# Optimization experiments

Measured on AMD Instinct MI355X. Metric: run time of the kernel, lower is better.

The kernel has to match this reference:

```python
import jax, jax.numpy as jnp
import numpy as np

B, L, D, H, I = 4, 1024, 2048, 16, 8192
DH = D // H  # 128
EPS = 1e-6


def setup_inputs() -> dict:
    key = jax.random.key(0)
    ks = jax.random.split(key, 10)
    hidden_states = jax.random.normal(ks[0], (B, L, D), dtype=jnp.float32)
    # additive causal mask [B,1,L,L]: 0 on allowed, large negative on masked
    causal = jnp.tril(jnp.ones((L, L), dtype=bool))
    attention_mask = jnp.where(causal, 0.0, -1e9).astype(jnp.float32)
    attention_mask = jnp.broadcast_to(attention_mask[None, None], (B, 1, L, L))
    # RoPE tables [B,L,DH]
    inv_freq = 1.0 / (10000.0 ** (jnp.arange(0, DH, 2, dtype=jnp.float32) / DH))
    pos = jnp.arange(L, dtype=jnp.float32)
    freqs = pos[:, None] * inv_freq[None, :]            # [L, DH/2]
    emb = jnp.concatenate([freqs, freqs], axis=-1)       # [L, DH]
    cos = jnp.broadcast_to(jnp.cos(emb)[None], (B, L, DH)).astype(jnp.float32)
    sin = jnp.broadcast_to(jnp.sin(emb)[None], (B, L, DH)).astype(jnp.float32)
    s = 0.02
    return {
        "hidden_states": hidden_states,
        "attention_mask": attention_mask,
        "cos": cos,
        "sin": sin,
        "q_w": jax.random.normal(ks[1], (D, D), jnp.float32) * s,
        "k_w": jax.random.normal(ks[2], (D, D), jnp.float32) * s,
        "v_w": jax.random.normal(ks[3], (D, D), jnp.float32) * s,
        "o_w": jax.random.normal(ks[4], (D, D), jnp.float32) * s,
        "gate_w": jax.random.normal(ks[5], (I, D), jnp.float32) * s,
        "up_w": jax.random.normal(ks[6], (I, D), jnp.float32) * s,
        "down_w": jax.random.normal(ks[7], (D, I), jnp.float32) * s,
        "ln1_w": jnp.ones((D,), jnp.float32),
        "ln2_w": jnp.ones((D,), jnp.float32),
    }


def _rms_norm(x, w):
    var = jnp.mean(jnp.square(x), axis=-1, keepdims=True)
    return x * jax.lax.rsqrt(var + EPS) * w


def _rotate_half(x):
    x1, x2 = jnp.split(x, 2, axis=-1)
    return jnp.concatenate([-x2, x1], axis=-1)


def reference(hidden_states, attention_mask, cos, sin, q_w, k_w, v_w, o_w,
              gate_w, up_w, down_w, ln1_w, ln2_w):
    residual = hidden_states
    h = _rms_norm(hidden_states, ln1_w)                       # [B,L,D]
    # QKV projections (torch Linear: x @ W^T)
    def heads(x, w):
        return (x @ w.T).reshape(B, L, H, DH).transpose(0, 2, 1, 3)  # [B,H,L,DH]
    q, k, v = heads(h, q_w), heads(h, k_w), heads(h, v_w)
    cos_b, sin_b = cos[:, None], sin[:, None]                 # [B,1,L,DH]
    q = q * cos_b + _rotate_half(q) * sin_b
    k = k * cos_b + _rotate_half(k) * sin_b
    scores = jnp.einsum('bhqd,bhkd->bhqk', q, k) / jnp.sqrt(jnp.float32(DH))
    scores = scores + attention_mask                          # [B,H,L,L]
    attn = jax.nn.softmax(scores, axis=-1)
    ctx = jnp.einsum('bhqk,bhkd->bhqd', attn, v)              # [B,H,L,DH]
    ctx = ctx.transpose(0, 2, 1, 3).reshape(B, L, D)
    attn_out = ctx @ o_w.T
    h1 = residual + attn_out
    h2 = _rms_norm(h1, ln2_w)
    mlp = (jax.nn.silu(h2 @ gate_w.T) * (h2 @ up_w.T)) @ down_w.T
    out = h1 + mlp
    return out, attn
```

## Files before the change

kernel.cpp:

```cpp
#include <hip/hip_runtime.h>


typedef __bf16 bf16;
typedef __bf16 bf16x8 __attribute__((ext_vector_type(8)));
typedef __bf16 bf16x4 __attribute__((ext_vector_type(4)));
typedef float  f32x4  __attribute__((ext_vector_type(4)));

constexpr int   kB  = 4;
constexpr int   kL  = 1024;
constexpr int   kD  = 2048;
constexpr int   kH  = 16;
constexpr int   kI  = 8192;
constexpr int   kDH = 128;
constexpr int   kQKV = 3 * kD;
constexpr float kEps = 1e-6f;
constexpr float kScoreScale = 0.08838834764831845f;

typedef __attribute__((address_space(1))) void gvoid_t;
typedef __attribute__((address_space(3))) void lvoid_t;

__device__ __forceinline__ void gload_lds16(const void* g, void* l) {
  __builtin_amdgcn_global_load_lds((gvoid_t*)g, (lvoid_t*)l, 16, 0, 0);
}

#define ASM_VMCNT(n) asm volatile("s_waitcnt vmcnt(" #n ")" ::: "memory")

__device__ __forceinline__ void bar_raw() {
  asm volatile("" ::: "memory");
  __builtin_amdgcn_s_barrier();
  asm volatile("" ::: "memory");
}

__global__ __launch_bounds__(256) void cast_f32_bf16_kernel(
    const float* __restrict__ x, bf16* __restrict__ y, long n) {
  long i = ((long)blockIdx.x * 256 + threadIdx.x) * 4;
  long stride = (long)gridDim.x * 256 * 4;
  for (; i < n; i += stride) {
    const float4 v = *reinterpret_cast<const float4*>(x + i);
    bf16x4 o;
    o[0] = (bf16)v.x; o[1] = (bf16)v.y; o[2] = (bf16)v.z; o[3] = (bf16)v.w;
    *reinterpret_cast<bf16x4*>(y + i) = o;
  }
}

__global__ __launch_bounds__(256) void rmsnorm_kernel(
    const float* __restrict__ x, const float* __restrict__ w,
    bf16* __restrict__ out) {
  const long row = blockIdx.x;
  const float* xr = x + row * (long)kD;
  bf16* orow = out + row * (long)kD;
  const int t = threadIdx.x;

  float4 v0 = *(const float4*)(xr + t * 8);
  float4 v1 = *(const float4*)(xr + t * 8 + 4);
  float ss = v0.x * v0.x + v0.y * v0.y + v0.z * v0.z + v0.w * v0.w +
             v1.x * v1.x + v1.y * v1.y + v1.z * v1.z + v1.w * v1.w;

  __shared__ float red[4];
  for (int off = 32; off > 0; off >>= 1) ss += __shfl_down(ss, off);
  if ((t & 63) == 0) red[t >> 6] = ss;
  __syncthreads();
  const float tot = red[0] + red[1] + red[2] + red[3];
  const float rs = rsqrtf(tot / (float)kD + kEps);

  float4 w0 = *(const float4*)(w + t * 8);
  float4 w1 = *(const float4*)(w + t * 8 + 4);
  bf16x8 o;
  o[0] = (bf16)(v0.x * rs * w0.x); o[1] = (bf16)(v0.y * rs * w0.y);
  o[2] = (bf16)(v0.z * rs * w0.z); o[3] = (bf16)(v0.w * rs * w0.w);
  o[4] = (bf16)(v1.x * rs * w1.x); o[5] = (bf16)(v1.y * rs * w1.y);
  o[6] = (bf16)(v1.z * rs * w1.z); o[7] = (bf16)(v1.w * rs * w1.w);
  *(bf16x8*)(orow + t * 8) = o;
}

__global__ __launch_bounds__(256) void rope_kernel(
    bf16* __restrict__ qkv, const float* __restrict__ cosb,
    const float* __restrict__ sinb) {
  const long row = blockIdx.x;
  const float* cr = cosb + row * (long)kDH;
  const float* sr = sinb + row * (long)kDH;
  bf16* qr = qkv + row * (long)kQKV;
  bf16* kr = qr + kD;
  const int t = threadIdx.x;
#pragma unroll
  for (int it = 0; it < 4; ++it) {
    const int p = it * 256 + t;
    const int h = p >> 6, i = p & 63;
    const int i0 = h * kDH + i, i1 = i0 + 64;
    const float c0 = cr[i], s0 = sr[i], c1 = cr[i + 64], s1 = sr[i + 64];
    const float q0 = (float)qr[i0], q1 = (float)qr[i1];
    qr[i0] = (bf16)(q0 * c0 - q1 * s0);
    qr[i1] = (bf16)(q1 * c1 + q0 * s1);
    const float k0 = (float)kr[i0], k1 = (float)kr[i1];
    kr[i0] = (bf16)(k0 * c0 - k1 * s0);
    kr[i1] = (bf16)(k1 * c1 + k0 * s1);
  }
}

__global__ __launch_bounds__(256) void transpose_v_kernel(
    const bf16* __restrict__ qkv, bf16* __restrict__ vT) {
  __shared__ bf16 tile[32][33];
  const int z = blockIdx.z, b = z / kH, h = z % kH;
  const bf16* src = qkv + (long)b * kL * kQKV + 2 * kD + h * kDH;
  bf16* dst = vT + (long)z * kDH * kL;
  const int l0 = blockIdx.x * 32, d0 = blockIdx.y * 32;
  const int tx = threadIdx.x & 31, ty = threadIdx.x >> 5;
  for (int r = ty; r < 32; r += 8)
    tile[r][tx] = src[(long)(l0 + r) * kQKV + d0 + tx];
  __syncthreads();
  for (int r = ty; r < 32; r += 8)
    dst[(long)(d0 + r) * kL + l0 + tx] = tile[tx][r];
}

__global__ __launch_bounds__(256) void merge_stats_kernel(
    const float2* __restrict__ sp, float2* __restrict__ sm) {
  const int idx = blockIdx.x * 256 + threadIdx.x;
  const int row = idx & 1023;
  const int n = ((row >> 7) + 1) * 2;
  const float2* p = sp + ((long)idx << 4);
  float M = -3.0e38f;
  for (int i = 0; i < n; ++i) M = fmaxf(M, p[i].x);
  float S = 0.f;
  for (int i = 0; i < n; ++i) S += p[i].y * expf(p[i].x - M);
  sm[idx] = make_float2(M, 1.0f / S);
}

enum { EPI_NONE = 0, EPI_ADD = 1, EPI_SILU = 3, EPI_OUTADD = 4,
       EPI_PASS1 = 6, EPI_PASS2 = 7 };

template <typename OutT, int EPI, bool AF32, int NF, bool CK>
__device__ __forceinline__ void gemm_body(
    const void* __restrict__ Ap, long sAo, long sAi, int lda,
    const bf16* __restrict__ Bp, long sBo, long sBi, int ldb,
    OutT* Cp, long sCo, long sCi, int ldc,
    const void* Ep, long sEo, long sEi, int lde,
    float scale, int Hdiv, int M, int N, int K) {
  constexpr int BN = 32 * NF;
  constexpr int ACH = 512;
  constexpr int BCH = BN * 4;
  static_assert((EPI != EPI_PASS1 && EPI != EPI_PASS2) || NF == 4, "pass NF=4");

  const int z = blockIdx.z;
  const int zo = z / Hdiv, zi = z % Hdiv;

  const bf16* A = nullptr;
  const float* Af = nullptr;
  if constexpr (AF32) Af = (const float*)Ap + zo * sAo + zi * sAi;
  else                A  = (const bf16*)Ap + zo * sAo + zi * sAi;
  const bf16* Bw = Bp + zo * sBo + zi * sBi;
  OutT* C = Cp + zo * sCo + zi * sCi;

  const int t = threadIdx.x;
  const int m0 = blockIdx.y * 128, n0 = blockIdx.x * BN;

  if constexpr (EPI == EPI_PASS1) {
    if (blockIdx.x > blockIdx.y) return;
  }
  if constexpr (EPI == EPI_PASS2) {
    if (blockIdx.x > blockIdx.y) {
      for (int e = t; e < 128 * 32; e += 256) {
        const int row = e >> 5, col = (e & 31) * 4;
        *(float4*)&C[(long)(m0 + row) * ldc + n0 + col] =
            make_float4(0.f, 0.f, 0.f, 0.f);
      }
      return;
    }
  }

  __shared__ __align__(16) bf16 lsA[2][128 * 32];
  __shared__ __align__(16) bf16 lsB[2][BN * 32];

  const int wave = t >> 6, lane = t & 63;
  const int wm = (wave >> 1) * 64, wn = (wave & 1) * (NF * 16);
  const int lr = lane & 15, lg = lane >> 4;

  f32x4 acc[4][NF] = {};

  auto stage = [&](int buf, int k0) {
    if constexpr (AF32) {
#pragma unroll
      for (int c = 0; c < 2; ++c) {
        const int id = c * 256 + t;
        const int row = id >> 2, col = (id & 3) * 8;
        const float* src = Af + (long)(m0 + row) * lda + k0 + col;
        const float4 u0 = *(const float4*)src;
        const float4 u1 = *(const float4*)(src + 4);
        bf16x8 wv;
        wv[0] = (bf16)u0.x; wv[1] = (bf16)u0.y; wv[2] = (bf16)u0.z; wv[3] = (bf16)u0.w;
        wv[4] = (bf16)u1.x; wv[5] = (bf16)u1.y; wv[6] = (bf16)u1.z; wv[7] = (bf16)u1.w;
        *(bf16x8*)&lsA[buf][id * 8] = wv;
        if (NF == 4 || c == 0)
          gload_lds16(Bw + (long)(n0 + row) * ldb + k0 + col, &lsB[buf][id * 8]);
      }
    } else {
#pragma unroll
      for (int c = 0; c < (ACH + BCH) / 256; ++c) {
        const int id = c * 256 + t;
        if (id < ACH) {
          const int row = id >> 2, col = (id & 3) * 8;
          gload_lds16(A + (long)(m0 + row) * lda + k0 + col, &lsA[buf][id * 8]);
        } else {
          const int fid = id - ACH;
          const int row = fid >> 2, col = (fid & 3) * 8;
          gload_lds16(Bw + (long)(n0 + row) * ldb + k0 + col, &lsB[buf][fid * 8]);
        }
      }
    }
  };

  auto compute = [&](int buf) {
    bf16x8 af[4], bfr[NF];
#pragma unroll
    for (int i = 0; i < 4; ++i)
      af[i] = *(const bf16x8*)&lsA[buf][(wm + i * 16 + lr) * 32 + lg * 8];
#pragma unroll
    for (int j = 0; j < NF; ++j)
      bfr[j] = *(const bf16x8*)&lsB[buf][(wn + j * 16 + lr) * 32 + lg * 8];
#pragma unroll
    for (int i = 0; i < 4; ++i)
#pragma unroll
      for (int j = 0; j < NF; ++j)
        acc[i][j] = __builtin_amdgcn_mfma_f32_16x16x32_bf16(af[i], bfr[j],
                                                            acc[i][j], 0, 0, 0);
  };

  const int Klim = CK ? (m0 + 128) : K;
  int cur = 0;

  if constexpr (AF32) {
    stage(0, 0);
    __syncthreads();
    for (int k0 = 0; k0 < Klim - 32; k0 += 32) {
      stage(cur ^ 1, k0 + 32);
      compute(cur);
      __syncthreads();
      cur ^= 1;
    }
    compute(cur);
  } else {
    stage(0, 0);
    for (int k0 = 0; k0 < Klim - 32; k0 += 32) {
      stage(cur ^ 1, k0 + 32);
      if constexpr (NF == 4) ASM_VMCNT(4); else ASM_VMCNT(3);
      bar_raw();
      compute(cur);
      bar_raw();
      cur ^= 1;
    }
    ASM_VMCNT(0);
    bar_raw();
    compute(cur);
  }

  if constexpr (EPI == EPI_PASS1) {
    float2* statsP = (float2*)Ep;
    const int half = wn >> 6, nt = blockIdx.x;
#pragma unroll
    for (int i = 0; i < 4; ++i) {
#pragma unroll
      for (int r = 0; r < 4; ++r) {
        const int rowg = m0 + wm + i * 16 + lg * 4 + r;
        float v[NF];
        float mx = -3.0e38f;
#pragma unroll
        for (int j = 0; j < NF; ++j) {
          const int colg = n0 + wn + j * 16 + lr;
          v[j] = acc[i][j][r] * scale + (colg > rowg ? -1.0e9f : 0.0f);
          mx = fmaxf(mx, v[j]);
        }
        for (int sh = 1; sh <= 8; sh <<= 1) mx = fmaxf(mx, __shfl_xor(mx, sh));
        float s = 0.f;
#pragma unroll
        for (int j = 0; j < NF; ++j) s += expf(v[j] - mx);
        for (int sh = 1; sh <= 8; sh <<= 1) s += __shfl_xor(s, sh);
        if (lr == 0)
          statsP[(((long)(z << 10) + rowg) << 4) + nt * 2 + half] =
              make_float2(mx, s);
      }
    }
  } else if constexpr (EPI == EPI_PASS2) {
    const float2* sm = (const float2*)Ep;
#pragma unroll
    for (int i = 0; i < 4; ++i) {
#pragma unroll
      for (int j = 0; j < NF; ++j) {
        const int colg = n0 + wn + j * 16 + lr;
#pragma unroll
        for (int r = 0; r < 4; ++r) {
          const int rowg = m0 + wm + i * 16 + lg * 4 + r;
          float p = 0.0f;
          if (colg <= rowg) {
            const float2 st = sm[(z << 10) + rowg];
            p = expf(acc[i][j][r] * scale - st.x) * st.y;
          }
          C[(long)rowg * ldc + colg] = (OutT)p;
        }
      }
    }
  } else {
    const float* Ef = (const float*)Ep;
    const bf16* Eb = (const bf16*)Ep;
    long ebase = 0;
    if constexpr (EPI == EPI_ADD || EPI == EPI_SILU)
      ebase = zo * sEo + zi * sEi;
#pragma unroll
    for (int i = 0; i < 4; ++i) {
#pragma unroll
      for (int j = 0; j < NF; ++j) {
        const int col = n0 + wn + j * 16 + lr;
#pragma unroll
        for (int r = 0; r < 4; ++r) {
          const int rowi = m0 + wm + i * 16 + lg * 4 + r;
          float val = acc[i][j][r] * scale;
          const long idx = (long)rowi * ldc + col;
          if constexpr (EPI == EPI_ADD)
            val += Ef[ebase + (long)rowi * lde + col];
          if constexpr (EPI == EPI_SILU) {
            const float g = (float)Eb[ebase + (long)rowi * lde + col];
            val = (g / (1.0f + expf(-g))) * val;
          }
          if constexpr (EPI == EPI_OUTADD)
            val += (float)C[idx];
          C[idx] = (OutT)val;
        }
      }
    }
  }
}

#define GEMM_ARGS                                                        \
  const void* __restrict__ Ap, long sAo, long sAi, int lda,              \
  const bf16* __restrict__ Bp, long sBo, long sBi, int ldb,              \
  void* Cp, long sCo, long sCi, int ldc,                                 \
  const void* Ep, long sEo, long sEi, int lde,                           \
  float scale, int Hdiv, int M, int N, int K
#define GEMM_PASS Ap, sAo, sAi, lda, Bp, sBo, sBi, ldb, (OUT_T*)Cp, sCo, \
  sCi, ldc, Ep, sEo, sEi, lde, scale, Hdiv, M, N, K

#define DEF_GEMM(NAME, OUT_TY, EPI_V, AF32_V, NF_V, CK_V)                \
  __global__ __launch_bounds__(256) void NAME(GEMM_ARGS) {               \
    using OUT_T = OUT_TY;                                                \
    gemm_body<OUT_T, EPI_V, AF32_V, NF_V, CK_V>(GEMM_PASS);              \
  }

DEF_GEMM(gemm_qkv,   bf16,  EPI_NONE,   false, 4, false)
DEF_GEMM(gemm_sc1,   float, EPI_PASS1,  false, 4, false)
DEF_GEMM(gemm_sc2,   float, EPI_PASS2,  false, 4, false)
DEF_GEMM(gemm_ctx,   bf16,  EPI_NONE,   true,  2, true)
DEF_GEMM(gemm_oproj, float, EPI_ADD,    false, 2, false)
DEF_GEMM(gemm_gate,  bf16,  EPI_NONE,   false, 4, false)
DEF_GEMM(gemm_up,    bf16,  EPI_SILU,   false, 4, false)
DEF_GEMM(gemm_down,  float, EPI_OUTADD, false, 2, false)

extern "C" void kernel_launch(void* const* d_in, const int* in_sizes, int n_in,
                              void* d_out, int out_size, void* d_ws,
                              size_t ws_size, hipStream_t stream) {
  (void)in_sizes; (void)n_in; (void)out_size; (void)ws_size;

  const float* hidden = (const float*)d_in[0];
  const float* cosb   = (const float*)d_in[2];
  const float* sinb   = (const float*)d_in[3];
  const float* q_w    = (const float*)d_in[4];
  const float* k_w    = (const float*)d_in[5];
  const float* v_w    = (const float*)d_in[6];
  const float* o_w    = (const float*)d_in[7];
  const float* gate_w = (const float*)d_in[8];
  const float* up_w   = (const float*)d_in[9];
  const float* down_w = (const float*)d_in[10];
  const float* ln1    = (const float*)d_in[11];
  const float* ln2    = (const float*)d_in[12];

  float* out  = (float*)d_out;
  float* attn = out + (long)kB * kL * kD;

  bf16* wsb = (bf16*)d_ws;
  long off = 0;
  bf16* WQKV = wsb + off; off += 3L * kD * kD;
  bf16* WO   = wsb + off; off += (long)kD * kD;
  bf16* WBIG = wsb + off; off += (long)kI * kD;
  bf16* HBF  = wsb + off; off += (long)kB * kL * kD;
  bf16* QKV  = wsb + off; off += (long)kB * kL * kQKV;
  bf16* GBUF = wsb + off; off += (long)kB * kL * kI;

  float2* STATS_P = (float2*)HBF;
  float2* STATS_M = STATS_P + (64L * 1024 * 16);

  const long DD = (long)kD * kD;
  const long ID = (long)kI * kD;
  const int  ML = kB * kL;

  cast_f32_bf16_kernel<<<dim3((int)(DD / 1024)), 256, 0, stream>>>(q_w, WQKV, DD);
  cast_f32_bf16_kernel<<<dim3((int)(DD / 1024)), 256, 0, stream>>>(k_w, WQKV + DD, DD);
  cast_f32_bf16_kernel<<<dim3((int)(DD / 1024)), 256, 0, stream>>>(v_w, WQKV + 2 * DD, DD);
  cast_f32_bf16_kernel<<<dim3((int)(DD / 1024)), 256, 0, stream>>>(o_w, WO, DD);

  rmsnorm_kernel<<<ML, 256, 0, stream>>>(hidden, ln1, HBF);

  gemm_qkv<<<dim3(kQKV / 128, ML / 128, 1), 256, 0, stream>>>(
      HBF, 0, 0, kD, WQKV, 0, 0, kD, QKV, 0, 0, kQKV,
      nullptr, 0, 0, 0, 1.0f, 1, ML, kQKV, kD);

  rope_kernel<<<ML, 256, 0, stream>>>(QKV, cosb, sinb);

  transpose_v_kernel<<<dim3(kL / 32, kDH / 32, kB * kH), 256, 0, stream>>>(QKV, GBUF);

  gemm_sc1<<<dim3(kL / 128, kL / 128, kB * kH), 256, 0, stream>>>(
      QKV, (long)kL * kQKV, kDH, kQKV,
      QKV + kD, (long)kL * kQKV, kDH, kQKV,
      attn, (long)kH * kL * kL, (long)kL * kL, kL,
      STATS_P, 0, 0, 0,
      kScoreScale, kH, kL, kL, kDH);

  merge_stats_kernel<<<256, 256, 0, stream>>>(STATS_P, STATS_M);

  gemm_sc2<<<dim3(kL / 128, kL / 128, kB * kH), 256, 0, stream>>>(
      QKV, (long)kL * kQKV, kDH, kQKV,
      QKV + kD, (long)kL * kQKV, kDH, kQKV,
      attn, (long)kH * kL * kL, (long)kL * kL, kL,
      STATS_M, 0, 0, 0,
      kScoreScale, kH, kL, kL, kDH);

  gemm_ctx<<<dim3(kDH / 64, kL / 128, kB * kH), 256, 0, stream>>>(
      attn, (long)kH * kL * kL, (long)kL * kL, kL,
      GBUF, (long)kH * kDH * kL, (long)kDH * kL, kL,
      HBF, (long)kL * kD, kDH, kD,
      nullptr, 0, 0, 0, 1.0f, kH, kL, kDH, kL);

  gemm_oproj<<<dim3(kD / 64, ML / 128, 1), 256, 0, stream>>>(
      HBF, 0, 0, kD, WO, 0, 0, kD, out, 0, 0, kD,
      hidden, 0, 0, kD, 1.0f, 1, ML, kD, kD);

  bf16* H2 = QKV;
  rmsnorm_kernel<<<ML, 256, 0, stream>>>(out, ln2, H2);

  cast_f32_bf16_kernel<<<dim3((int)(ID / 1024)), 256, 0, stream>>>(gate_w, WBIG, ID);
  gemm_gate<<<dim3(kI / 128, ML / 128, 1), 256, 0, stream>>>(
      H2, 0, 0, kD, WBIG, 0, 0, kD, GBUF, 0, 0, kI,
      nullptr, 0, 0, 0, 1.0f, 1, ML, kI, kD);

  cast_f32_bf16_kernel<<<dim3((int)(ID / 1024)), 256, 0, stream>>>(up_w, WBIG, ID);
  gemm_up<<<dim3(kI / 128, ML / 128, 1), 256, 0, stream>>>(
      H2, 0, 0, kD, WBIG, 0, 0, kD, GBUF, 0, 0, kI,
      GBUF, 0, 0, kI, 1.0f, 1, ML, kI, kD);

  cast_f32_bf16_kernel<<<dim3((int)(ID / 1024)), 256, 0, stream>>>(down_w, WBIG, ID);
  gemm_down<<<dim3(kD / 64, ML / 128, 1), 256, 0, stream>>>(
      GBUF, 0, 0, kI, WBIG, 0, 0, kI, out, 0, 0, kD,
      nullptr, 0, 0, 0, 1.0f, 1, ML, kD, kI);
}
```

Before: 1.153 ms.

## Add 256x256-tile triple-buffered GEMM for QKV, gate and up projections

Introduces a new 512-thread GEMM kernel with 256x256 output tiles, an 8x4 MFMA fragment per wave, and a three-stage LDS pipeline fed by direct global-to-LDS loads. It replaces the 128x128 generic GEMM for the QKV, gate and up projections, and the SiLU-multiply epilogue moves into the new kernel. Larger tiles raise arithmetic intensity and cut redundant global loads. The cost is heavy register pressure (128 accumulator floats per lane), about 96KB of LDS, and fewer blocks, which can limit occupancy and tail efficiency.

```diff
diff --git a/kernel.cpp b/kernel.cpp
--- a/kernel.cpp
+++ b/kernel.cpp
@@ -125,8 +125,90 @@
   sm[idx] = make_float2(M, 1.0f / S);
 }
 
-enum { EPI_NONE = 0, EPI_ADD = 1, EPI_SILU = 3, EPI_OUTADD = 4,
-       EPI_PASS1 = 6, EPI_PASS2 = 7 };
+template <int EPI>
+__global__ __launch_bounds__(512) void gemm256_body(
+    const bf16* __restrict__ A, int lda, const bf16* __restrict__ B, int ldb,
+    bf16* __restrict__ C, int ldc, const bf16* __restrict__ Ep, int lde,
+    int K) {
+  constexpr int NBUF = 3;
+  __shared__ __align__(16) bf16 lsA[NBUF][256 * 32];
+  __shared__ __align__(16) bf16 lsB[NBUF][256 * 32];
+
+  const int t = threadIdx.x;
+  const int m0 = blockIdx.x * 256, n0 = blockIdx.y * 256;
+  const int wave = t >> 6, lane = t & 63;
+  const int wm = (wave >> 2) * 128, wn = (wave & 3) * 64;
+  const int lr = lane & 15, lg = lane >> 4;
+
+  f32x4 acc[8][4] = {};
+
+  auto stage = [&](int buf, int k0) {
+#pragma unroll
+    for (int c = 0; c < 2; ++c) {
+      const int id = c * 512 + t;
+      const int row = id >> 2, col = (id & 3) * 8;
+      gload_lds16(A + (long)(m0 + row) * lda + k0 + col, &lsA[buf][id * 8]);
+      gload_lds16(B + (long)(n0 + row) * ldb + k0 + col, &lsB[buf][id * 8]);
+    }
+  };
+
+  auto compute = [&](int buf) {
+    bf16x8 af[8], bfr[4];
+#pragma unroll
+    for (int i = 0; i < 8; ++i)
+      af[i] = *(const bf16x8*)&lsA[buf][(wm + i * 16 + lr) * 32 + lg * 8];
+#pragma unroll
+    for (int j = 0; j < 4; ++j)
+      bfr[j] = *(const bf16x8*)&lsB[buf][(wn + j * 16 + lr) * 32 + lg * 8];
+#pragma unroll
+    for (int i = 0; i < 8; ++i)
+#pragma unroll
+      for (int j = 0; j < 4; ++j)
+        acc[i][j] = __builtin_amdgcn_mfma_f32_16x16x32_bf16(af[i], bfr[j],
+                                                            acc[i][j], 0, 0, 0);
+  };
+
+  stage(0, 0);
+  stage(1, 32);
+  int cur = 0, k0 = 0;
+  for (; k0 + 64 < K; k0 += 32) {
+    const int nxt = cur == 2 ? 0 : cur + 1;
+    const int pre = nxt == 2 ? 0 : nxt + 1;
+    stage(pre, k0 + 64);
+    ASM_VMCNT(8);
+    bar_raw();
+    compute(cur);
+    bar_raw();
+    cur = nxt;
+  }
+  ASM_VMCNT(4);
+  bar_raw();
+  compute(cur);
+  cur = cur == 2 ? 0 : cur + 1;
+  ASM_VMCNT(0);
+  bar_raw();
+  compute(cur);
+
+#pragma unroll
+  for (int i = 0; i < 8; ++i) {
+#pragma unroll
+    for (int j = 0; j < 4; ++j) {
+      const int col = n0 + wn + j * 16 + lr;
+#pragma unroll
+      for (int r = 0; r < 4; ++r) {
+        const int row = m0 + wm + i * 16 + lg * 4 + r;
+        float val = acc[i][j][r];
+        if constexpr (EPI == 3) {
+          const float g = (float)Ep[(long)row * lde + col];
+          val = (g / (1.0f + expf(-g))) * val;
+        }
+        C[(long)row * ldc + col] = (bf16)val;
+      }
+    }
+  }
+}
+
+enum { EPI_NONE = 0, EPI_ADD = 1, EPI_OUTADD = 4, EPI_PASS1 = 6, EPI_PASS2 = 7 };
 
 template <typename OutT, int EPI, bool AF32, int NF, bool CK>
 __device__ __forceinline__ void gemm_body(
@@ -299,9 +381,8 @@
     }
   } else {
     const float* Ef = (const float*)Ep;
-    const bf16* Eb = (const bf16*)Ep;
     long ebase = 0;
-    if constexpr (EPI == EPI_ADD || EPI == EPI_SILU)
+    if constexpr (EPI == EPI_ADD)
       ebase = zo * sEo + zi * sEi;
 #pragma unroll
     for (int i = 0; i < 4; ++i) {
@@ -315,10 +396,6 @@
           const long idx = (long)rowi * ldc + col;
           if constexpr (EPI == EPI_ADD)
             val += Ef[ebase + (long)rowi * lde + col];
-          if constexpr (EPI == EPI_SILU) {
-            const float g = (float)Eb[ebase + (long)rowi * lde + col];
-            val = (g / (1.0f + expf(-g))) * val;
-          }
           if constexpr (EPI == EPI_OUTADD)
             val += (float)C[idx];
           C[idx] = (OutT)val;
@@ -343,13 +420,10 @@
     gemm_body<OUT_T, EPI_V, AF32_V, NF_V, CK_V>(GEMM_PASS);              \
   }
 
-DEF_GEMM(gemm_qkv,   bf16,  EPI_NONE,   false, 4, false)
 DEF_GEMM(gemm_sc1,   float, EPI_PASS1,  false, 4, false)
 DEF_GEMM(gemm_sc2,   float, EPI_PASS2,  false, 4, false)
 DEF_GEMM(gemm_ctx,   bf16,  EPI_NONE,   true,  2, true)
 DEF_GEMM(gemm_oproj, float, EPI_ADD,    false, 2, false)
-DEF_GEMM(gemm_gate,  bf16,  EPI_NONE,   false, 4, false)
-DEF_GEMM(gemm_up,    bf16,  EPI_SILU,   false, 4, false)
 DEF_GEMM(gemm_down,  float, EPI_OUTADD, false, 2, false)
 
 extern "C" void kernel_launch(void* const* d_in, const int* in_sizes, int n_in,
@@ -396,9 +470,8 @@
 
   rmsnorm_kernel<<<ML, 256, 0, stream>>>(hidden, ln1, HBF);
 
-  gemm_qkv<<<dim3(kQKV / 128, ML / 128, 1), 256, 0, stream>>>(
-      HBF, 0, 0, kD, WQKV, 0, 0, kD, QKV, 0, 0, kQKV,
-      nullptr, 0, 0, 0, 1.0f, 1, ML, kQKV, kD);
+  gemm256_body<0><<<dim3(ML / 256, kQKV / 256), 512, 0, stream>>>(
+      HBF, kD, WQKV, kD, QKV, kQKV, nullptr, 0, kD);
 
   rope_kernel<<<ML, 256, 0, stream>>>(QKV, cosb, sinb);
 
@@ -434,14 +507,12 @@
   rmsnorm_kernel<<<ML, 256, 0, stream>>>(out, ln2, H2);
 
   cast_f32_bf16_kernel<<<dim3((int)(ID / 1024)), 256, 0, stream>>>(gate_w, WBIG, ID);
-  gemm_gate<<<dim3(kI / 128, ML / 128, 1), 256, 0, stream>>>(
-      H2, 0, 0, kD, WBIG, 0, 0, kD, GBUF, 0, 0, kI,
-      nullptr, 0, 0, 0, 1.0f, 1, ML, kI, kD);
+  gemm256_body<0><<<dim3(ML / 256, kI / 256), 512, 0, stream>>>(
+      H2, kD, WBIG, kD, GBUF, kI, nullptr, 0, kD);
 
   cast_f32_bf16_kernel<<<dim3((int)(ID / 1024)), 256, 0, stream>>>(up_w, WBIG, ID);
-  gemm_up<<<dim3(kI / 128, ML / 128, 1), 256, 0, stream>>>(
-      H2, 0, 0, kD, WBIG, 0, 0, kD, GBUF, 0, 0, kI,
-      GBUF, 0, 0, kI, 1.0f, 1, ML, kI, kD);
+  gemm256_body<3><<<dim3(ML / 256, kI / 256), 512, 0, stream>>>(
+      H2, kD, WBIG, kD, GBUF, kI, GBUF, kI, kD);
 
   cast_f32_bf16_kernel<<<dim3((int)(ID / 1024)), 256, 0, stream>>>(down_w, WBIG, ID);
   gemm_down<<<dim3(kD / 64, ML / 128, 1), 256, 0, stream>>>(
```

Result: no change. 1.143 ms (-0.8%).
